# Kernel tuning notes

Hardware: AMD Instinct MI355X
Metric: run time of the kernel (lower is better)

## Reference

```python
import jax, jax.numpy as jnp
import numpy as np
import math

B, IN_CH, IMG = 32, 3, 128
D, L, H, MLP, P = 512, 8, 8, 2048, 8
HD = D // H
EPS = 1e-5


def _conv(x, w, b, stride, pad):
    y = jax.lax.conv_general_dilated(x, w, (stride, stride), pad,
                                     dimension_numbers=("NCHW", "OIHW", "NCHW"))
    return y + b[None, :, None, None]


def _gn(x, g, b, groups):
    Bn, C, Hh, W = x.shape
    xr = x.reshape(Bn, groups, C // groups, Hh, W)
    m = jnp.mean(xr, axis=(2, 3, 4), keepdims=True)
    v = jnp.var(xr, axis=(2, 3, 4), keepdims=True)
    xr = (xr - m) / jnp.sqrt(v + EPS)
    return xr.reshape(Bn, C, Hh, W) * g[None, :, None, None] + b[None, :, None, None]


def _ln(x, g, b):
    m = jnp.mean(x, axis=-1, keepdims=True)
    v = jnp.var(x, axis=-1, keepdims=True)
    return (x - m) / jnp.sqrt(v + EPS) * g + b


def _rot_half(x):
    # interleaved pairs: (x0,x1) -> (-x1,x0)
    x1, x2 = x[..., 0::2], x[..., 1::2]
    return jnp.stack((-x2, x1), axis=-1).reshape(x.shape)


def _xpos_tables(n_pos, hd):
    # faithful to rotary_embedding_torch with use_xpos=True, scale_base=512
    inv = 1.0 / (10000.0 ** (jnp.arange(0, hd, 2, dtype=jnp.float32) / hd))
    seq = jnp.arange(n_pos, dtype=jnp.float32)
    freqs = jnp.repeat(seq[:, None] * inv[None, :], 2, axis=-1)  # (n_pos, hd) interleaved
    sv = (jnp.arange(0, hd, 2, dtype=jnp.float32) + 0.4 * hd) / (1.4 * hd)
    power = (seq - n_pos // 2) / 512.0
    scale = sv[None, :] ** power[:, None]                        # (n_pos, hd//2)
    scale = jnp.concatenate([scale, scale], axis=-1)             # library uses cat, not interleave
    return jnp.cos(freqs), jnp.sin(freqs), scale


def _pos2d(N, Dd):
    g = int(math.isqrt(N))
    y = jnp.tile(jnp.arange(g), g).astype(jnp.float32)
    x = jnp.repeat(jnp.arange(g), g).astype(jnp.float32)
    dq = Dd // 4
    omega = jnp.exp(jnp.arange(dq, dtype=jnp.float32) * -(math.log(10000.0) / dq))
    px, py = x[:, None] * omega, y[:, None] * omega
    return jnp.concatenate([jnp.sin(px), jnp.cos(px), jnp.sin(py), jnp.cos(py)], axis=-1)[None]


def setup_inputs() -> dict:
    key = jax.random.key(0)
    ks = iter(jax.random.split(key, 40))
    def rn(shape, s=0.02):
        return jax.random.normal(next(ks), shape, jnp.float32) * s
    return dict(
        x=jax.random.normal(next(ks), (B, IN_CH, IMG, IMG), jnp.float32),
        conv1_w=rn((32, 3, 3, 3)), conv1_b=jnp.zeros((32,), jnp.float32),
        gn1_g=jnp.ones((32,), jnp.float32), gn1_b=jnp.zeros((32,), jnp.float32),
        conv2_w=rn((64, 32, 3, 3)), conv2_b=jnp.zeros((64,), jnp.float32),
        gn2_g=jnp.ones((64,), jnp.float32), gn2_b=jnp.zeros((64,), jnp.float32),
        patch_w=rn((D, 64, P, P)), patch_b=jnp.zeros((D,), jnp.float32),
        cls_token=rn((1, 1, D), 1.0),
        ln1_g=jnp.ones((L, D), jnp.float32), ln1_b=jnp.zeros((L, D), jnp.float32),
        qkv_w=rn((L, D, 3 * D)), qkv_b=jnp.zeros((L, 3 * D), jnp.float32),
        out_w=rn((L, D, D)), out_b=jnp.zeros((L, D), jnp.float32),
        ln2_g=jnp.ones((L, D), jnp.float32), ln2_b=jnp.zeros((L, D), jnp.float32),
        w1_w=rn((L, D, MLP)), w1_b=jnp.zeros((L, MLP), jnp.float32),
        w2_w=rn((L, D, MLP)), w2_b=jnp.zeros((L, MLP), jnp.float32),
        w3_w=rn((L, MLP, D)), w3_b=jnp.zeros((L, D), jnp.float32),
        fn_g=jnp.ones((D,), jnp.float32), fn_b=jnp.zeros((D,), jnp.float32),
    )


def _forward(x, conv1_w, conv1_b, gn1_g, gn1_b, conv2_w, conv2_b, gn2_g, gn2_b,
             patch_w, patch_b, cls_token, ln1_g, ln1_b, qkv_w, qkv_b, out_w, out_b,
             ln2_g, ln2_b, w1_w, w1_b, w2_w, w2_b, w3_w, w3_b, fn_g, fn_b):
    # conv stem (no downsample)
    f = jax.nn.gelu(_gn(_conv(x, conv1_w, conv1_b, 1, [(1, 1), (1, 1)]), gn1_g, gn1_b, 4), approximate=False)
    f = jax.nn.gelu(_gn(_conv(f, conv2_w, conv2_b, 1, [(1, 1), (1, 1)]), gn2_g, gn2_b, 8), approximate=False)
    # patch embed
    p = _conv(f, patch_w, patch_b, P, "VALID")            # (B, D, g, g)
    Bn, Dd, gh, gw = p.shape
    tokens = p.reshape(Bn, Dd, gh * gw).transpose(0, 2, 1)  # (B, N, D)
    tokens = tokens + _pos2d(gh * gw, Dd)
    xa = jnp.concatenate([jnp.broadcast_to(cls_token, (Bn, 1, Dd)), tokens], axis=1)
    # NOTE: original code applies RoPE with seq_dim=-2 on (B,S,H,hd) -> rotation indexed by HEAD axis
    cos, sin, xsc = _xpos_tables(H, HD)
    scale_att = HD ** -0.5
    for i in range(L):
        n = _ln(xa, ln1_g[i], ln1_b[i])
        qkv = (n @ qkv_w[i] + qkv_b[i]).reshape(Bn, -1, 3, H, HD)
        q, k, v = qkv[:, :, 0], qkv[:, :, 1], qkv[:, :, 2]     # (B, S, H, hd)
        q = q * cos * xsc + _rot_half(q) * sin * xsc
        k = k * cos / xsc + _rot_half(k) * sin / xsc
        attn = jax.nn.softmax(jnp.einsum("bihd,bjhd->bhij", q, k) * scale_att, axis=-1)
        y = jnp.einsum("bhij,bjhd->bihd", attn, v).reshape(Bn, -1, Dd)
        xa = xa + y @ out_w[i] + out_b[i]
        n2 = _ln(xa, ln2_g[i], ln2_b[i])
        xa = xa + (jax.nn.silu(n2 @ w1_w[i] + w1_b[i]) * (n2 @ w2_w[i] + w2_b[i])) @ w3_w[i] + w3_b[i]
    return _ln(xa, fn_g, fn_b)


def reference(x, conv1_w, conv1_b, gn1_g, gn1_b, conv2_w, conv2_b, gn2_g, gn2_b,
              patch_w, patch_b, cls_token, ln1_g, ln1_b, qkv_w, qkv_b, out_w, out_b,
              ln2_g, ln2_b, w1_w, w1_b, w2_w, w2_b, w3_w, w3_b, fn_g, fn_b):
    xa = _forward(x, conv1_w, conv1_b, gn1_g, gn1_b, conv2_w, conv2_b, gn2_g, gn2_b,
                  patch_w, patch_b, cls_token, ln1_g, ln1_b, qkv_w, qkv_b, out_w, out_b,
                  ln2_g, ln2_b, w1_w, w1_b, w2_w, w2_b, w3_w, w3_b, fn_g, fn_b)
    return (xa[:, 0], xa[:, 1:])  # (cls, patches); grid_hw is static (16,16)
```

## Files before the change

### kernel.cpp

```cpp
#include <hip/hip_runtime.h>

#define EPSV 1e-5f
typedef unsigned short u16;
typedef short bf16x8 __attribute__((ext_vector_type(8)));
typedef float f32x4 __attribute__((ext_vector_type(4)));

__device__ __forceinline__ float gelu_exact(float x) {
    return 0.5f * x * (1.0f + erff(x * 0.7071067811865475f));
}
__device__ __forceinline__ u16 to_bf(float x) {
    union { float f; unsigned u; } c; c.f = x;
    unsigned r = c.u + 0x7fffu + ((c.u >> 16) & 1u);
    return (u16)(r >> 16);
}
__device__ __forceinline__ float to_f(u16 h) {
    union { unsigned u; float f; } c; c.u = ((unsigned)h) << 16;
    return c.f;
}
__device__ __forceinline__ void gload_lds16(const void* g, void* l) {
    __builtin_amdgcn_global_load_lds((const __attribute__((address_space(1))) unsigned int*)g,
                                     (__attribute__((address_space(3))) unsigned int*)l, 16, 0, 0);
}

__global__ void k_wsfail(float* out) { out[0] = 1.0e9f; }

__global__ void k_zero(float* p, int n) {
    int i = blockIdx.x * 256 + threadIdx.x;
    if (i < n) p[i] = 0.0f;
}

__global__ void k_wt(const float* __restrict__ w, float* __restrict__ wt, int cout, int cin9) {
    int idx = blockIdx.x * 256 + threadIdx.x;
    if (idx < cout * cin9) {
        int co = idx / cin9, k = idx % cin9;
        wt[k * cout + co] = w[idx];
    }
}

__global__ void k_wpack(const float* __restrict__ w, u16* __restrict__ wp) {
    int idx = blockIdx.x * 256 + threadIdx.x;
    if (idx < 18432) {
        int ci = idx & 31, tc = idx >> 5;
        int tap = tc >> 6, co = tc & 63;
        wp[idx] = to_bf(w[co * 288 + ci * 9 + tap]);
    }
}

__global__ void k_pperm(const float* __restrict__ w, u16* __restrict__ wp) {
    int idx = blockIdx.x * 256 + threadIdx.x;
    int cout = idx >> 12, rem = idx & 4095;
    int tap = rem >> 6, ci = rem & 63;
    wp[idx] = to_bf(w[cout * 4096 + ci * 64 + tap]);
}

__global__ void k_biascat(const float* __restrict__ b1, const float* __restrict__ b2,
                          float* __restrict__ o) {
    int idx = blockIdx.x * 256 + threadIdx.x;
    if (idx < 32768) {
        int l = idx >> 12, pc = idx & 4095;
        int chunk = pc >> 4, within = pc & 15;
        int srccol = (chunk >> 1) * 16 + within;
        o[idx] = (chunk & 1) ? b2[l * 2048 + srccol] : b1[l * 2048 + srccol];
    }
}

__global__ void k_tables(float* __restrict__ postab, float* __restrict__ ropetab) {
    int idx = blockIdx.x * 256 + threadIdx.x;
    if (idx < 256 * 512) {
        int p = idx >> 9, j = idx & 511;
        float coord = (j < 256) ? (float)(p >> 4) : (float)(p & 15);
        int jm = j & 127;
        float om = powf(10000.0f, -(float)jm / 128.0f);
        float arg = coord * om;
        postab[idx] = ((j >> 7) & 1) ? cosf(arg) : sinf(arg);
    }
    if (idx < 512) {
        int h = idx >> 6, d = idx & 63;
        float freq = (float)h * powf(10000.0f, -(float)(d >> 1) / 32.0f);
        float sv = (2.0f * (float)(d & 31) + 25.6f) / 89.6f;
        float pw = ((float)h - 4.0f) / 512.0f;
        float sc = powf(sv, pw);
        ropetab[idx * 4 + 0] = cosf(freq);
        ropetab[idx * 4 + 1] = sinf(freq);
        ropetab[idx * 4 + 2] = sc * 0.125f;
        ropetab[idx * 4 + 3] = 1.0f / sc;
    }
}

__global__ void k_cls(const float* __restrict__ cls, float* __restrict__ xa) {
    int idx = blockIdx.x * 256 + threadIdx.x;
    int b = idx >> 9, d = idx & 511;
    xa[(size_t)(b * 257) * 512 + d] = cls[d];
}

__global__ __launch_bounds__(256) void k_wcvtT(const float* __restrict__ src,
                                               u16* __restrict__ dst, int K, int N) {
    __shared__ float s[32][33];
    int z = blockIdx.z;
    src += (size_t)z * K * N;
    dst += (size_t)z * K * N;
    int k0 = blockIdx.y * 32, n0 = blockIdx.x * 32;
    int t = threadIdx.x, r = t >> 3, c4 = (t & 7) * 4;
    float4 v = *(const float4*)&src[(size_t)(k0 + r) * N + n0 + c4];
    s[r][c4 + 0] = v.x; s[r][c4 + 1] = v.y; s[r][c4 + 2] = v.z; s[r][c4 + 3] = v.w;
    __syncthreads();
    ushort4 o;
    o.x = to_bf(s[c4 + 0][r]); o.y = to_bf(s[c4 + 1][r]);
    o.z = to_bf(s[c4 + 2][r]); o.w = to_bf(s[c4 + 3][r]);
    *(ushort4*)&dst[(size_t)(n0 + r) * K + k0 + c4] = o;
}

__global__ __launch_bounds__(256) void k_wcvtT12(const float* __restrict__ s1,
                                                 const float* __restrict__ s2,
                                                 u16* __restrict__ dst, int K, int N) {
    __shared__ float s[32][33];
    int z = blockIdx.z;
    const float* src = z ? s2 : s1;
    int k0 = blockIdx.y * 32, n0 = blockIdx.x * 32;
    int t = threadIdx.x, r = t >> 3, c4 = (t & 7) * 4;
    float4 v = *(const float4*)&src[(size_t)(k0 + r) * N + n0 + c4];
    s[r][c4 + 0] = v.x; s[r][c4 + 1] = v.y; s[r][c4 + 2] = v.z; s[r][c4 + 3] = v.w;
    __syncthreads();
    ushort4 o;
    o.x = to_bf(s[c4 + 0][r]); o.y = to_bf(s[c4 + 1][r]);
    o.z = to_bf(s[c4 + 2][r]); o.w = to_bf(s[c4 + 3][r]);
    int nsrc = n0 + r;
    int p = ((nsrc >> 4) << 5) + (z << 4) + (nsrc & 15);
    *(ushort4*)&dst[(size_t)p * K + k0 + c4] = o;
}

__global__ __launch_bounds__(256) void k_conv1(const float* __restrict__ in,
                                               const float* __restrict__ wt,
                                               const float* __restrict__ bias,
                                               u16* __restrict__ f1n,
                                               float* __restrict__ sacc) {
    __shared__ float s_in[3][18][18];
    __shared__ float rs[4][4], rq[4][4];
    int b = blockIdx.y;
    int tile = blockIdx.x;
    int y0 = (tile >> 3) << 4;
    int x0 = (tile & 7) << 4;
    int tid = threadIdx.x;
    for (int idx = tid; idx < 972; idx += 256) {
        int ci = idx / 324, r = idx % 324;
        int ly = r / 18, lx = r % 18;
        int gy = y0 + ly - 1, gx = x0 + lx - 1;
        float v = 0.0f;
        if (gy >= 0 && gy < 128 && gx >= 0 && gx < 128)
            v = in[((size_t)(b * 3 + ci) * 128 + gy) * 128 + gx];
        s_in[ci][ly][lx] = v;
    }
    __syncthreads();
    int py = tid >> 4, px = tid & 15;
    float acc[32];
#pragma unroll
    for (int co = 0; co < 32; co++) acc[co] = bias[co];
#pragma unroll
    for (int ci = 0; ci < 3; ci++)
#pragma unroll
        for (int dy = 0; dy < 3; dy++)
#pragma unroll
            for (int dx = 0; dx < 3; dx++) {
                float v = s_in[ci][py + dy][px + dx];
                const float* wr = &wt[(ci * 9 + dy * 3 + dx) * 32];
#pragma unroll
                for (int co = 0; co < 32; co++)
                    acc[co] = fmaf(wr[co], v, acc[co]);
            }
    float s[4] = {0.f, 0.f, 0.f, 0.f}, q[4] = {0.f, 0.f, 0.f, 0.f};
    u16 ob[32];
#pragma unroll
    for (int co = 0; co < 32; co++) {
        u16 hv = to_bf(acc[co]);
        ob[co] = hv;
        float v = to_f(hv);
        s[co >> 3] += v;
        q[co >> 3] += v * v;
    }
    int oy = y0 + py, ox = x0 + px;
    u16* dst = f1n + ((size_t)(b * 16384 + oy * 128 + ox) << 5);
#pragma unroll
    for (int i = 0; i < 8; i++)
        *(ushort4*)(dst + i * 4) = make_ushort4(ob[i * 4], ob[i * 4 + 1], ob[i * 4 + 2], ob[i * 4 + 3]);
#pragma unroll
    for (int g = 0; g < 4; g++) {
#pragma unroll
        for (int off = 1; off < 64; off <<= 1) {
            s[g] += __shfl_xor(s[g], off);
            q[g] += __shfl_xor(q[g], off);
        }
    }
    int w = tid >> 6, lane = tid & 63;
    if (lane == 0)
#pragma unroll
        for (int g = 0; g < 4; g++) { rs[g][w] = s[g]; rq[g][w] = q[g]; }
    __syncthreads();
    if (tid < 4) {
        int g = tid;
        float S = rs[g][0] + rs[g][1] + rs[g][2] + rs[g][3];
        float Q = rq[g][0] + rq[g][1] + rq[g][2] + rq[g][3];
        atomicAdd(&sacc[(b * 4 + g) * 2], S);
        atomicAdd(&sacc[(b * 4 + g) * 2 + 1], Q);
    }
}

__global__ void k_gnfin(const float* __restrict__ sacc, float* __restrict__ st, int entries) {
    int i = blockIdx.x * 256 + threadIdx.x;
    if (i < entries) {
        float m = sacc[2 * i] * (1.0f / 131072.0f);
        float var = sacc[2 * i + 1] * (1.0f / 131072.0f) - m * m;
        st[2 * i] = m;
        st[2 * i + 1] = rsqrtf(var + 1e-5f);
    }
}

__global__ void k_gnap(u16* __restrict__ xio, const float* __restrict__ st,
                       const float* __restrict__ gg, const float* __restrict__ bb,
                       int cm, int sh, int gmul) {
    int idx = blockIdx.x * 256 + threadIdx.x;
    long e = (long)idx * 4;
    int c0 = (int)(e & cm);
    int b = (int)(e >> sh);
    int sid = b * gmul + (c0 >> 3);
    float m = st[2 * sid], r = st[2 * sid + 1];
    ushort4 a = *(ushort4*)&xio[e];
    ushort4 o;
    o.x = to_bf(gelu_exact((to_f(a.x) - m) * r * gg[c0 + 0] + bb[c0 + 0]));
    o.y = to_bf(gelu_exact((to_f(a.y) - m) * r * gg[c0 + 1] + bb[c0 + 1]));
    o.z = to_bf(gelu_exact((to_f(a.z) - m) * r * gg[c0 + 2] + bb[c0 + 2]));
    o.w = to_bf(gelu_exact((to_f(a.w) - m) * r * gg[c0 + 3] + bb[c0 + 3]));
    *(ushort4*)&xio[e] = o;
}

__global__ __launch_bounds__(256) void k_conv2m(const u16* __restrict__ f1b,
                                                const u16* __restrict__ wp,
                                                const float* __restrict__ bias,
                                                u16* __restrict__ f2n,
                                                float* __restrict__ sacc) {
    int b = blockIdx.y;
    int tile = blockIdx.x;
    int y0 = (tile >> 3) << 4;
    int x0 = (tile & 7) << 4;
    int tid = threadIdx.x;
    int w = tid >> 6, lane = tid & 63;
    int l15 = lane & 15, l16 = lane >> 4;

    const u16* base = f1b + ((size_t)b << 19);

    f32x4 acc[4][4];
    f32x4 zf = {0.f, 0.f, 0.f, 0.f};
#pragma unroll
    for (int m = 0; m < 4; m++)
#pragma unroll
        for (int n = 0; n < 4; n++) acc[m][n] = zf;
    bf16x8 zb = {0, 0, 0, 0, 0, 0, 0, 0};

#pragma unroll
    for (int tap = 0; tap < 9; tap++) {
        int dy = tap / 3, dx = tap % 3;
        int gx = x0 + l15 + dx - 1;
        bf16x8 af[4], bk[4];
#pragma unroll
        for (int m = 0; m < 4; m++) {
            int gy = y0 + w * 4 + m + dy - 1;
            bool ok = (gy >= 0) && (gy < 128) && (gx >= 0) && (gx < 128);
            int pix = ok ? (gy * 128 + gx) : 0;
            bf16x8 v = *(const bf16x8*)(base + ((size_t)pix << 5) + l16 * 8);
            af[m] = ok ? v : zb;
        }
#pragma unroll
        for (int n = 0; n < 4; n++)
            bk[n] = *(const bf16x8*)&wp[(tap * 64 + n * 16 + l15) * 32 + l16 * 8];
#pragma unroll
        for (int m = 0; m < 4; m++)
#pragma unroll
            for (int n = 0; n < 4; n++)
                acc[m][n] = __builtin_amdgcn_mfma_f32_16x16x32_bf16(af[m], bk[n], acc[m][n], 0, 0, 0);
    }

#pragma unroll
    for (int n = 0; n < 4; n++) {
        int gco = n * 16 + l15;
        float bv = bias[gco];
        float sn = 0.0f, qn = 0.0f;
#pragma unroll
        for (int m = 0; m < 4; m++) {
            int py = w * 4 + m;
#pragma unroll
            for (int r = 0; r < 4; r++) {
                int px = l16 * 4 + r;
                float v = acc[m][n][r] + bv;
                u16 hv = to_bf(v);
                f2n[((size_t)(b * 16384 + (y0 + py) * 128 + x0 + px) << 6) + gco] = hv;
                float vf = to_f(hv);
                sn += vf;
                qn += vf * vf;
            }
        }
#pragma unroll
        for (int off = 1; off <= 4; off <<= 1) { sn += __shfl_xor(sn, off); qn += __shfl_xor(qn, off); }
        sn += __shfl_xor(sn, 16); qn += __shfl_xor(qn, 16);
        sn += __shfl_xor(sn, 32); qn += __shfl_xor(qn, 32);
        if (lane == 0 || lane == 8) {
            int g = n * 2 + (lane >> 3);
            atomicAdd(&sacc[(b * 8 + g) * 2], sn);
            atomicAdd(&sacc[(b * 8 + g) * 2 + 1], qn);
        }
    }
}

template <int MODE, int EPI>
__global__ __launch_bounds__(256) void k_bgemm(const u16* __restrict__ A,
                                               const u16* __restrict__ Bt,
                                               const float* __restrict__ bias,
                                               void* __restrict__ Cp,
                                               const float* __restrict__ aux,
                                               int M, int N, int K) {
    __shared__ u16 ldsA[8192];
    __shared__ u16 ldsB[8192];
    int tid = threadIdx.x;
    int w = tid >> 6, lane = tid & 63;
    int bm = blockIdx.y * 128, bn = blockIdx.x * 128;
    int wr = w >> 1, wc = w & 1;
    int l15 = lane & 15, l16 = lane >> 4;

    f32x4 acc[4][4];
    f32x4 zf = {0.f, 0.f, 0.f, 0.f};
#pragma unroll
    for (int m = 0; m < 4; m++)
#pragma unroll
        for (int n = 0; n < 4; n++) acc[m][n] = zf;

    for (int k0 = 0; k0 < K; k0 += 64) {
#pragma unroll
        for (int i = 0; i < 4; i++) {
            int chunk = (w * 4 + i) * 64 + lane;
            int kg = chunk >> 7, row = chunk & 127;
            const u16* src;
            if (MODE == 0) {
                int grow = bm + row;
                if (grow > M - 1) grow = M - 1;
                src = A + (size_t)grow * K + k0 + kg * 8;
            } else {
                int grow = bm + row;
                int bimg = grow >> 8, p = grow & 255;
                int kga = (k0 >> 3) + kg;
                int tap = kga >> 3, cq = kga & 7;
                int ky = tap >> 3, kx = tap & 7;
                int gy = ((p >> 4) << 3) + ky, gx = ((p & 15) << 3) + kx;
                src = A + (((size_t)(bimg * 16384 + gy * 128 + gx)) << 6) + cq * 8;
            }
            gload_lds16(src, &ldsA[(w * 4 + i) * 512]);
        }
#pragma unroll
        for (int i = 0; i < 4; i++) {
            int chunk = (w * 4 + i) * 64 + lane;
            int col = chunk >> 3, kgs = chunk & 7;
            int kg_src = kgs ^ (col & 7);
            const u16* src = Bt + (size_t)(bn + col) * K + k0 + kg_src * 8;
            gload_lds16(src, &ldsB[(w * 4 + i) * 512]);
        }
        __syncthreads();

        bf16x8 af[4][2], bfr[4][2];
#pragma unroll
        for (int kk = 0; kk < 2; kk++) {
            int kga = kk * 4 + l16;
#pragma unroll
            for (int m = 0; m < 4; m++) {
                int row_l = wr * 64 + m * 16 + l15;
                af[m][kk] = *(const bf16x8*)&ldsA[(kga * 128 + row_l) * 8];
            }
#pragma unroll
            for (int n = 0; n < 4; n++) {
                int col_l = wc * 64 + n * 16 + l15;
                bfr[n][kk] = *(const bf16x8*)&ldsB[(col_l * 8 + (kga ^ (col_l & 7))) * 8];
            }
        }
#pragma unroll
        for (int m = 0; m < 4; m++)
#pragma unroll
            for (int n = 0; n < 4; n++) {
                acc[m][n] = __builtin_amdgcn_mfma_f32_16x16x32_bf16(af[m][0], bfr[n][0], acc[m][n], 0, 0, 0);
                acc[m][n] = __builtin_amdgcn_mfma_f32_16x16x32_bf16(af[m][1], bfr[n][1], acc[m][n], 0, 0, 0);
            }
        __syncthreads();
    }

    if (EPI == 6) {
#pragma unroll
        for (int np = 0; np < 2; np++) {
            int n_a = np * 2, n_b = np * 2 + 1;
            float bva = bias[bn + wc * 64 + n_a * 16 + l15];
            float bvb = bias[bn + wc * 64 + n_b * 16 + l15];
            int ocol = (bn >> 1) + wc * 32 + np * 16 + l15;
#pragma unroll
            for (int m = 0; m < 4; m++) {
#pragma unroll
                for (int r = 0; r < 4; r++) {
                    int grow = bm + wr * 64 + m * 16 + l16 * 4 + r;
                    if (grow < M) {
                        float h1v = to_f(to_bf(acc[m][n_a][r] + bva));
                        float h2v = to_f(to_bf(acc[m][n_b][r] + bvb));
                        float sl = h1v / (1.0f + __expf(-h1v));
                        ((u16*)Cp)[(size_t)grow * (N >> 1) + ocol] = to_bf(sl * h2v);
                    }
                }
            }
        }
    } else {
#pragma unroll
        for (int n = 0; n < 4; n++) {
            int gcol = bn + wc * 64 + n * 16 + l15;
            float bv = bias[gcol];
            float rc = 0.f, rsn = 0.f, rsc = 1.f;
            bool isqk = false, odd = false;
            if (EPI == 7) {
                isqk = gcol < 1024;
                odd = (l15 & 1) != 0;
                const float* rb = &aux[(gcol & 511) * 4];
                if (isqk) {
                    rc = rb[0]; rsn = rb[1];
                    rsc = (gcol < 512) ? rb[2] : rb[3];
                }
            }
#pragma unroll
            for (int m = 0; m < 4; m++) {
#pragma unroll
                for (int r = 0; r < 4; r++) {
                    int grow = bm + wr * 64 + m * 16 + l16 * 4 + r;
                    float v = acc[m][n][r] + bv;
                    if (EPI == 7) {
                        float p = __shfl_xor(v, 1);
                        float vr = isqk ? ((odd ? (v * rc + p * rsn) : (v * rc - p * rsn)) * rsc) : v;
                        if (grow < M) ((u16*)Cp)[(size_t)grow * N + gcol] = to_bf(vr);
                    } else if (EPI == 1) {
                        if (grow < M) ((float*)Cp)[(size_t)grow * N + gcol] = v;
                    } else if (EPI == 2) {
                        if (grow < M) ((float*)Cp)[(size_t)grow * N + gcol] += v;
                    } else {
                        int bimg = grow >> 8, p2 = grow & 255;
                        v += aux[p2 * 512 + gcol];
                        ((float*)Cp)[((size_t)(bimg * 257) + 1 + p2) * 512 + gcol] = v;
                    }
                }
            }
        }
    }
}

__global__ __launch_bounds__(256) void k_lnb(const float* __restrict__ x,
                                             const float* __restrict__ g,
                                             const float* __restrict__ bta,
                                             u16* __restrict__ o) {
    int row = blockIdx.x * 4 + (threadIdx.x >> 6);
    int lane = threadIdx.x & 63;
    const float4* xr = (const float4*)(x + (size_t)row * 512);
    float4 a = xr[lane * 2], b = xr[lane * 2 + 1];
    float s = a.x + a.y + a.z + a.w + b.x + b.y + b.z + b.w;
#pragma unroll
    for (int off = 1; off < 64; off <<= 1) s += __shfl_xor(s, off);
    float mean = s * (1.0f / 512.0f);
    float d[8] = {a.x - mean, a.y - mean, a.z - mean, a.w - mean,
                  b.x - mean, b.y - mean, b.z - mean, b.w - mean};
    float q = 0.0f;
#pragma unroll
    for (int i = 0; i < 8; i++) q += d[i] * d[i];
#pragma unroll
    for (int off = 1; off < 64; off <<= 1) q += __shfl_xor(q, off);
    float rstd = rsqrtf(q * (1.0f / 512.0f) + EPSV);
    int c0 = lane * 8;
    float4 g0 = *(const float4*)&g[c0], g1 = *(const float4*)&g[c0 + 4];
    float4 b0 = *(const float4*)&bta[c0], b1 = *(const float4*)&bta[c0 + 4];
    u16* orow = o + (size_t)row * 512 + c0;
    *(ushort4*)orow = make_ushort4(to_bf(d[0] * rstd * g0.x + b0.x), to_bf(d[1] * rstd * g0.y + b0.y),
                                   to_bf(d[2] * rstd * g0.z + b0.z), to_bf(d[3] * rstd * g0.w + b0.w));
    *(ushort4*)(orow + 4) = make_ushort4(to_bf(d[4] * rstd * g1.x + b1.x), to_bf(d[5] * rstd * g1.y + b1.y),
                                         to_bf(d[6] * rstd * g1.z + b1.z), to_bf(d[7] * rstd * g1.w + b1.w));
}

__global__ __launch_bounds__(256) void k_ln_out(const float* __restrict__ x,
                                                const float* __restrict__ g,
                                                const float* __restrict__ bta,
                                                float* __restrict__ out) {
    int row = blockIdx.x * 4 + (threadIdx.x >> 6);
    int lane = threadIdx.x & 63;
    const float4* xr = (const float4*)(x + (size_t)row * 512);
    float4 a = xr[lane * 2], b = xr[lane * 2 + 1];
    float s = a.x + a.y + a.z + a.w + b.x + b.y + b.z + b.w;
#pragma unroll
    for (int off = 1; off < 64; off <<= 1) s += __shfl_xor(s, off);
    float mean = s * (1.0f / 512.0f);
    float d[8] = {a.x - mean, a.y - mean, a.z - mean, a.w - mean,
                  b.x - mean, b.y - mean, b.z - mean, b.w - mean};
    float q = 0.0f;
#pragma unroll
    for (int i = 0; i < 8; i++) q += d[i] * d[i];
#pragma unroll
    for (int off = 1; off < 64; off <<= 1) q += __shfl_xor(q, off);
    float rstd = rsqrtf(q * (1.0f / 512.0f) + EPSV);
    int bb = row / 257, t = row % 257;
    float* dst = (t == 0) ? out + (size_t)bb * 512
                          : out + 16384 + (size_t)(bb * 256 + (t - 1)) * 512;
    int c0 = lane * 8;
    float4 g0 = *(const float4*)&g[c0], g1 = *(const float4*)&g[c0 + 4];
    float4 b0 = *(const float4*)&bta[c0], b1 = *(const float4*)&bta[c0 + 4];
    *(float4*)(dst + c0) = make_float4(d[0] * rstd * g0.x + b0.x, d[1] * rstd * g0.y + b0.y,
                                       d[2] * rstd * g0.z + b0.z, d[3] * rstd * g0.w + b0.w);
    *(float4*)(dst + c0 + 4) = make_float4(d[4] * rstd * g1.x + b1.x, d[5] * rstd * g1.y + b1.y,
                                           d[6] * rstd * g1.z + b1.z, d[7] * rstd * g1.w + b1.w);
}

__global__ __launch_bounds__(256) void k_attn_mfma(const u16* __restrict__ qkv,
                                                   u16* __restrict__ y) {
    __shared__ u16 KV[64][72];
    __shared__ float sc[32][260];
    __shared__ u16 Pb[32][328];
    __shared__ float red1[32][8];
    __shared__ float red2[32][8];
    __shared__ float invr[32];

    int bid = blockIdx.x;
    int qt = bid % 9, bh = bid / 9;
    int h = bh & 7, b = bh >> 3;
    int q0 = qt * 32;
    int tid = threadIdx.x;
    int w = tid >> 6, lane = tid & 63;
    int l15 = lane & 15, l16 = lane >> 4;

    bf16x8 aq[2][2];
#pragma unroll
    for (int m = 0; m < 2; m++) {
        int grow = q0 + m * 16 + l15; if (grow > 256) grow = 256;
        const u16* qp = qkv + (size_t)(b * 257 + grow) * 1536 + h * 64 + l16 * 8;
        aq[m][0] = *(const bf16x8*)qp;
        aq[m][1] = *(const bf16x8*)(qp + 32);
    }

    for (int t = 0; t < 5; t++) {
        int j0 = t * 64;
        int gk = j0 + w * 16 + l15; if (gk > 256) gk = 256;
        const u16* kp = qkv + (size_t)(b * 257 + gk) * 1536 + 512 + h * 64 + l16 * 8;
        bf16x8 bk0 = *(const bf16x8*)kp;
        bf16x8 bk1 = *(const bf16x8*)(kp + 32);
        f32x4 a2[2];
        f32x4 zf = {0.f, 0.f, 0.f, 0.f};
#pragma unroll
        for (int m = 0; m < 2; m++) {
            a2[m] = zf;
            a2[m] = __builtin_amdgcn_mfma_f32_16x16x32_bf16(aq[m][0], bk0, a2[m], 0, 0, 0);
            a2[m] = __builtin_amdgcn_mfma_f32_16x16x32_bf16(aq[m][1], bk1, a2[m], 0, 0, 0);
        }
        int col = j0 + w * 16 + l15;
        if (col < 257) {
#pragma unroll
            for (int m = 0; m < 2; m++)
#pragma unroll
                for (int r = 0; r < 4; r++)
                    sc[m * 16 + l16 * 4 + r][col] = a2[m][r];
        }
    }
    __syncthreads();

    {
        int r = tid >> 3, sub = tid & 7;
        float mx = -1e30f;
        for (int j = sub; j < 257; j += 8) mx = fmaxf(mx, sc[r][j]);
        red1[r][sub] = mx;
        __syncthreads();
        mx = red1[r][0];
#pragma unroll
        for (int i = 1; i < 8; i++) mx = fmaxf(mx, red1[r][i]);
        float sm = 0.0f;
        for (int j = sub; j < 257; j += 8) {
            float e = __expf(sc[r][j] - mx);
            Pb[r][j] = to_bf(e);
            sm += e;
        }
        for (int j = 257 + sub; j < 320; j += 8) Pb[r][j] = 0;
        red2[r][sub] = sm;
        __syncthreads();
        if (sub == 0) {
            float t = red2[r][0];
#pragma unroll
            for (int i = 1; i < 8; i++) t += red2[r][i];
            invr[r] = 1.0f / t;
        }
        __syncthreads();
    }

    f32x4 oacc[2];
    {
        f32x4 zf = {0.f, 0.f, 0.f, 0.f};
        oacc[0] = zf; oacc[1] = zf;
    }
    for (int t = 0; t < 5; t++) {
        int j0 = t * 64;
        {
            int vk = tid & 63, vd0 = (tid >> 6) * 16;
            int gk = j0 + vk;
            u16 o[16];
            if (gk <= 256) {
                const u16* vp = qkv + (size_t)(b * 257 + gk) * 1536 + 1024 + h * 64 + vd0;
                ushort4 a0 = *(const ushort4*)vp, a1 = *(const ushort4*)(vp + 4);
                ushort4 a2v = *(const ushort4*)(vp + 8), a3 = *(const ushort4*)(vp + 12);
                o[0] = a0.x; o[1] = a0.y; o[2] = a0.z; o[3] = a0.w;
                o[4] = a1.x; o[5] = a1.y; o[6] = a1.z; o[7] = a1.w;
                o[8] = a2v.x; o[9] = a2v.y; o[10] = a2v.z; o[11] = a2v.w;
                o[12] = a3.x; o[13] = a3.y; o[14] = a3.z; o[15] = a3.w;
            } else {
#pragma unroll
                for (int i = 0; i < 16; i++) o[i] = 0;
            }
#pragma unroll
            for (int i = 0; i < 16; i++) KV[vd0 + i][vk] = o[i];
        }
        __syncthreads();

        bf16x8 ap[2][2], bv[2];
#pragma unroll
        for (int m = 0; m < 2; m++)
#pragma unroll
            for (int kk = 0; kk < 2; kk++)
                ap[m][kk] = *(const bf16x8*)&Pb[m * 16 + l15][j0 + kk * 32 + l16 * 8];
#pragma unroll
        for (int kk = 0; kk < 2; kk++)
            bv[kk] = *(const bf16x8*)&KV[w * 16 + l15][kk * 32 + l16 * 8];
#pragma unroll
        for (int m = 0; m < 2; m++) {
            oacc[m] = __builtin_amdgcn_mfma_f32_16x16x32_bf16(ap[m][0], bv[0], oacc[m], 0, 0, 0);
            oacc[m] = __builtin_amdgcn_mfma_f32_16x16x32_bf16(ap[m][1], bv[1], oacc[m], 0, 0, 0);
        }
        __syncthreads();
    }

#pragma unroll
    for (int m = 0; m < 2; m++)
#pragma unroll
        for (int r = 0; r < 4; r++) {
            int lr = m * 16 + l16 * 4 + r;
            int grow = q0 + lr;
            if (grow < 257)
                y[(size_t)(b * 257 + grow) * 512 + h * 64 + w * 16 + l15] =
                    to_bf(oacc[m][r] * invr[lr]);
        }
}

extern "C" void kernel_launch(void* const* d_in, const int* in_sizes, int n_in,
                              void* d_out, int out_size, void* d_ws, size_t ws_size,
                              hipStream_t stream) {
    const float* x       = (const float*)d_in[0];
    const float* conv1_w = (const float*)d_in[1];
    const float* conv1_b = (const float*)d_in[2];
    const float* gn1_g   = (const float*)d_in[3];
    const float* gn1_b   = (const float*)d_in[4];
    const float* conv2_w = (const float*)d_in[5];
    const float* conv2_b = (const float*)d_in[6];
    const float* gn2_g   = (const float*)d_in[7];
    const float* gn2_b   = (const float*)d_in[8];
    const float* patch_w = (const float*)d_in[9];
    const float* patch_b = (const float*)d_in[10];
    const float* cls_tok = (const float*)d_in[11];
    const float* ln1_g   = (const float*)d_in[12];
    const float* ln1_b   = (const float*)d_in[13];
    const float* qkv_w   = (const float*)d_in[14];
    const float* qkv_b   = (const float*)d_in[15];
    const float* out_w   = (const float*)d_in[16];
    const float* out_b   = (const float*)d_in[17];
    const float* ln2_g   = (const float*)d_in[18];
    const float* ln2_b   = (const float*)d_in[19];
    const float* w1_w    = (const float*)d_in[20];
    const float* w1_b    = (const float*)d_in[21];
    const float* w2_w    = (const float*)d_in[22];
    const float* w2_b    = (const float*)d_in[23];
    const float* w3_w    = (const float*)d_in[24];
    const float* w3_b    = (const float*)d_in[25];
    const float* fn_g    = (const float*)d_in[26];
    const float* fn_b    = (const float*)d_in[27];
    float* out = (float*)d_out;
    char* wsb  = (char*)d_ws;

    const size_t O_R1    = 0;
    const size_t O_HB    = O_R1 + 67371008;
    const size_t O_NB    = O_R1 + 101056512;
    const size_t O_Y     = O_R1 + 109477888;
    const size_t O_R2    = 134217728;
    const size_t O_XA    = 201326592;
    const size_t O_PWT   = 218169344;
    const size_t O_QKVT  = 222363648;
    const size_t O_OUTT  = 234946560;
    const size_t O_WL    = 239140864;
    const size_t O_PT    = 245432320;
    const size_t O_RT    = 245956608;
    const size_t O_CW1   = 245964800;
    const size_t O_CW2   = 245968896;
    const size_t O_ST    = 246042624;
    const size_t O_SA    = 246046720;
    const size_t O_B12   = 246050816;
    const size_t NEED    = 246181888;
    if (ws_size < NEED) {
        k_wsfail<<<1, 1, 0, stream>>>(out);
        return;
    }
    u16*   f2n    = (u16*)(wsb + O_R1);
    u16*   hb     = (u16*)(wsb + O_HB);
    u16*   nb     = (u16*)(wsb + O_NB);
    u16*   yb     = (u16*)(wsb + O_Y);
    u16*   f1n    = (u16*)(wsb + O_R2);
    u16*   qkvb   = (u16*)(wsb + O_R2);
    float* xa     = (float*)(wsb + O_XA);
    u16*   patchT = (u16*)(wsb + O_PWT);
    u16*   qkvT   = (u16*)(wsb + O_QKVT);
    u16*   outT   = (u16*)(wsb + O_OUTT);
    u16*   w12Tl  = (u16*)(wsb + O_WL);
    u16*   w3Tl   = (u16*)(wsb + O_WL + 4194304);
    float* postab = (float*)(wsb + O_PT);
    float* ropet  = (float*)(wsb + O_RT);
    float* w1t    = (float*)(wsb + O_CW1);
    u16*   wpack  = (u16*)(wsb + O_CW2);
    float* stat   = (float*)(wsb + O_ST);
    float* sacc   = (float*)(wsb + O_SA);
    float* bias12 = (float*)(wsb + O_B12);

    k_zero<<<3, 256, 0, stream>>>(sacc, 768);
    k_wt<<<4, 256, 0, stream>>>(conv1_w, w1t, 32, 27);
    k_wpack<<<72, 256, 0, stream>>>(conv2_w, wpack);
    k_tables<<<512, 256, 0, stream>>>(postab, ropet);
    k_pperm<<<8192, 256, 0, stream>>>(patch_w, patchT);
    k_biascat<<<128, 256, 0, stream>>>(w1_b, w2_b, bias12);
    k_wcvtT<<<dim3(48, 16, 8), 256, 0, stream>>>(qkv_w, qkvT, 512, 1536);
    k_wcvtT<<<dim3(16, 16, 8), 256, 0, stream>>>(out_w, outT, 512, 512);

    k_conv1<<<dim3(64, 32), 256, 0, stream>>>(x, w1t, conv1_b, f1n, sacc);
    k_gnfin<<<1, 256, 0, stream>>>(sacc, stat, 128);
    k_gnap<<<16384, 256, 0, stream>>>(f1n, stat, gn1_g, gn1_b, 31, 19, 4);
    k_conv2m<<<dim3(64, 32), 256, 0, stream>>>(f1n, wpack, conv2_b, f2n, sacc + 256);
    k_gnfin<<<1, 256, 0, stream>>>(sacc + 256, stat + 256, 256);
    k_gnap<<<32768, 256, 0, stream>>>(f2n, stat + 256, gn2_g, gn2_b, 63, 20, 8);

    k_bgemm<1, 3><<<dim3(4, 64), 256, 0, stream>>>(f2n, patchT, patch_b, xa, postab, 8192, 512, 4096);
    k_cls<<<64, 256, 0, stream>>>(cls_tok, xa);

    for (int l = 0; l < 8; l++) {
        k_wcvtT12<<<dim3(64, 16, 2), 256, 0, stream>>>(w1_w + (size_t)l * 1048576,
                                                       w2_w + (size_t)l * 1048576, w12Tl, 512, 2048);
        k_wcvtT<<<dim3(16, 64, 1), 256, 0, stream>>>(w3_w + (size_t)l * 1048576, w3Tl, 2048, 512);

        k_lnb<<<2056, 256, 0, stream>>>(xa, ln1_g + l * 512, ln1_b + l * 512, nb);
        k_bgemm<0, 7><<<dim3(12, 65), 256, 0, stream>>>(nb, qkvT + (size_t)l * 786432,
                                                        qkv_b + l * 1536, qkvb, ropet, 8224, 1536, 512);
        k_attn_mfma<<<2304, 256, 0, stream>>>(qkvb, yb);
        k_bgemm<0, 2><<<dim3(4, 65), 256, 0, stream>>>(yb, outT + (size_t)l * 262144,
                                                       out_b + l * 512, xa, nullptr, 8224, 512, 512);
        k_lnb<<<2056, 256, 0, stream>>>(xa, ln2_g + l * 512, ln2_b + l * 512, nb);
        k_bgemm<0, 6><<<dim3(32, 65), 256, 0, stream>>>(nb, w12Tl,
                                                        bias12 + l * 4096, hb, nullptr, 8224, 4096, 512);
        k_bgemm<0, 2><<<dim3(4, 65), 256, 0, stream>>>(hb, w3Tl,
                                                       w3_b + l * 512, xa, nullptr, 8224, 512, 2048);
    }
    k_ln_out<<<2056, 256, 0, stream>>>(xa, fn_g, fn_b, out);
}
```

Measured before the change: 2.596 ms.

## Merge setup kernels, batch MLP weight conversion, double-buffer attention V tile

```diff
diff --git a/kernel.cpp b/kernel.cpp
--- a/kernel.cpp
+++ b/kernel.cpp
@@ -24,49 +24,15 @@
 
 __global__ void k_wsfail(float* out) { out[0] = 1.0e9f; }
 
-__global__ void k_zero(float* p, int n) {
-    int i = blockIdx.x * 256 + threadIdx.x;
-    if (i < n) p[i] = 0.0f;
-}
-
-__global__ void k_wt(const float* __restrict__ w, float* __restrict__ wt, int cout, int cin9) {
+__global__ void k_setup(float* __restrict__ sacc,
+                        const float* __restrict__ conv1_w, float* __restrict__ w1t,
+                        const float* __restrict__ conv2_w, u16* __restrict__ wpack,
+                        const float* __restrict__ b1, const float* __restrict__ b2,
+                        float* __restrict__ bias12,
+                        float* __restrict__ postab, float* __restrict__ ropetab,
+                        const float* __restrict__ cls, float* __restrict__ xa) {
     int idx = blockIdx.x * 256 + threadIdx.x;
-    if (idx < cout * cin9) {
-        int co = idx / cin9, k = idx % cin9;
-        wt[k * cout + co] = w[idx];
-    }
-}
-
-__global__ void k_wpack(const float* __restrict__ w, u16* __restrict__ wp) {
-    int idx = blockIdx.x * 256 + threadIdx.x;
-    if (idx < 18432) {
-        int ci = idx & 31, tc = idx >> 5;
-        int tap = tc >> 6, co = tc & 63;
-        wp[idx] = to_bf(w[co * 288 + ci * 9 + tap]);
-    }
-}
-
-__global__ void k_pperm(const float* __restrict__ w, u16* __restrict__ wp) {
-    int idx = blockIdx.x * 256 + threadIdx.x;
-    int cout = idx >> 12, rem = idx & 4095;
-    int tap = rem >> 6, ci = rem & 63;
-    wp[idx] = to_bf(w[cout * 4096 + ci * 64 + tap]);
-}
-
-__global__ void k_biascat(const float* __restrict__ b1, const float* __restrict__ b2,
-                          float* __restrict__ o) {
-    int idx = blockIdx.x * 256 + threadIdx.x;
-    if (idx < 32768) {
-        int l = idx >> 12, pc = idx & 4095;
-        int chunk = pc >> 4, within = pc & 15;
-        int srccol = (chunk >> 1) * 16 + within;
-        o[idx] = (chunk & 1) ? b2[l * 2048 + srccol] : b1[l * 2048 + srccol];
-    }
-}
-
-__global__ void k_tables(float* __restrict__ postab, float* __restrict__ ropetab) {
-    int idx = blockIdx.x * 256 + threadIdx.x;
-    if (idx < 256 * 512) {
+    if (idx < 131072) {
         int p = idx >> 9, j = idx & 511;
         float coord = (j < 256) ? (float)(p >> 4) : (float)(p & 15);
         int jm = j & 127;
@@ -85,12 +51,33 @@
         ropetab[idx * 4 + 2] = sc * 0.125f;
         ropetab[idx * 4 + 3] = 1.0f / sc;
     }
-}
-
-__global__ void k_cls(const float* __restrict__ cls, float* __restrict__ xa) {
+    if (idx < 768) sacc[idx] = 0.0f;
+    if (idx < 864) {
+        int co = idx / 27, k = idx % 27;
+        w1t[k * 32 + co] = conv1_w[idx];
+    }
+    if (idx < 18432) {
+        int ci = idx & 31, tc = idx >> 5;
+        int tap = tc >> 6, co = tc & 63;
+        wpack[idx] = to_bf(conv2_w[co * 288 + ci * 9 + tap]);
+    }
+    if (idx < 32768) {
+        int l = idx >> 12, pc = idx & 4095;
+        int chunk = pc >> 4, within = pc & 15;
+        int srccol = (chunk >> 1) * 16 + within;
+        bias12[idx] = (chunk & 1) ? b2[l * 2048 + srccol] : b1[l * 2048 + srccol];
+    }
+    if (idx < 16384) {
+        int b = idx >> 9, d = idx & 511;
+        xa[(size_t)(b * 257) * 512 + d] = cls[d];
+    }
+}
+
+__global__ void k_pperm(const float* __restrict__ w, u16* __restrict__ wp) {
     int idx = blockIdx.x * 256 + threadIdx.x;
-    int b = idx >> 9, d = idx & 511;
-    xa[(size_t)(b * 257) * 512 + d] = cls[d];
+    int cout = idx >> 12, rem = idx & 4095;
+    int tap = rem >> 6, ci = rem & 63;
+    wp[idx] = to_bf(w[cout * 4096 + ci * 64 + tap]);
 }
 
 __global__ __launch_bounds__(256) void k_wcvtT(const float* __restrict__ src,
@@ -110,23 +97,25 @@
     *(ushort4*)&dst[(size_t)(n0 + r) * K + k0 + c4] = o;
 }
 
-__global__ __launch_bounds__(256) void k_wcvtT12(const float* __restrict__ s1,
-                                                 const float* __restrict__ s2,
-                                                 u16* __restrict__ dst, int K, int N) {
+__global__ __launch_bounds__(256) void k_wcvtT12L(const float* __restrict__ w1,
+                                                  const float* __restrict__ w2,
+                                                  u16* __restrict__ w12All) {
     __shared__ float s[32][33];
     int z = blockIdx.z;
-    const float* src = z ? s2 : s1;
+    int layer = z >> 1, sel = z & 1;
+    const float* src = (sel ? w2 : w1) + (size_t)layer * 1048576;
+    u16* dst = w12All + (size_t)layer * 2097152;
     int k0 = blockIdx.y * 32, n0 = blockIdx.x * 32;
     int t = threadIdx.x, r = t >> 3, c4 = (t & 7) * 4;
-    float4 v = *(const float4*)&src[(size_t)(k0 + r) * N + n0 + c4];
+    float4 v = *(const float4*)&src[(size_t)(k0 + r) * 2048 + n0 + c4];
     s[r][c4 + 0] = v.x; s[r][c4 + 1] = v.y; s[r][c4 + 2] = v.z; s[r][c4 + 3] = v.w;
     __syncthreads();
     ushort4 o;
     o.x = to_bf(s[c4 + 0][r]); o.y = to_bf(s[c4 + 1][r]);
     o.z = to_bf(s[c4 + 2][r]); o.w = to_bf(s[c4 + 3][r]);
     int nsrc = n0 + r;
-    int p = ((nsrc >> 4) << 5) + (z << 4) + (nsrc & 15);
-    *(ushort4*)&dst[(size_t)p * K + k0 + c4] = o;
+    int p = ((nsrc >> 4) << 5) + (sel << 4) + (nsrc & 15);
+    *(ushort4*)&dst[(size_t)p * 512 + k0 + c4] = o;
 }
 
 __global__ __launch_bounds__(256) void k_conv1(const float* __restrict__ in,
@@ -204,17 +193,7 @@
     }
 }
 
-__global__ void k_gnfin(const float* __restrict__ sacc, float* __restrict__ st, int entries) {
-    int i = blockIdx.x * 256 + threadIdx.x;
-    if (i < entries) {
-        float m = sacc[2 * i] * (1.0f / 131072.0f);
-        float var = sacc[2 * i + 1] * (1.0f / 131072.0f) - m * m;
-        st[2 * i] = m;
-        st[2 * i + 1] = rsqrtf(var + 1e-5f);
-    }
-}
-
-__global__ void k_gnap(u16* __restrict__ xio, const float* __restrict__ st,
+__global__ void k_gnap(u16* __restrict__ xio, const float* __restrict__ sacc,
                        const float* __restrict__ gg, const float* __restrict__ bb,
                        int cm, int sh, int gmul) {
     int idx = blockIdx.x * 256 + threadIdx.x;
@@ -222,7 +201,9 @@
     int c0 = (int)(e & cm);
     int b = (int)(e >> sh);
     int sid = b * gmul + (c0 >> 3);
-    float m = st[2 * sid], r = st[2 * sid + 1];
+    float m = sacc[2 * sid] * (1.0f / 131072.0f);
+    float var = sacc[2 * sid + 1] * (1.0f / 131072.0f) - m * m;
+    float r = rsqrtf(var + 1e-5f);
     ushort4 a = *(ushort4*)&xio[e];
     ushort4 o;
     o.x = to_bf(gelu_exact((to_f(a.x) - m) * r * gg[c0 + 0] + bb[c0 + 0]));
@@ -513,7 +494,7 @@
 
 __global__ __launch_bounds__(256) void k_attn_mfma(const u16* __restrict__ qkv,
                                                    u16* __restrict__ y) {
-    __shared__ u16 KV[64][72];
+    __shared__ u16 KV[2][64][72];
     __shared__ float sc[32][260];
     __shared__ u16 Pb[32][328];
     __shared__ float red1[32][8];
@@ -596,6 +577,7 @@
     }
     for (int t = 0; t < 5; t++) {
         int j0 = t * 64;
+        int buf = t & 1;
         {
             int vk = tid & 63, vd0 = (tid >> 6) * 16;
             int gk = j0 + vk;
@@ -613,7 +595,7 @@
                 for (int i = 0; i < 16; i++) o[i] = 0;
             }
 #pragma unroll
-            for (int i = 0; i < 16; i++) KV[vd0 + i][vk] = o[i];
+            for (int i = 0; i < 16; i++) KV[buf][vd0 + i][vk] = o[i];
         }
         __syncthreads();
 
@@ -625,13 +607,12 @@
                 ap[m][kk] = *(const bf16x8*)&Pb[m * 16 + l15][j0 + kk * 32 + l16 * 8];
 #pragma unroll
         for (int kk = 0; kk < 2; kk++)
-            bv[kk] = *(const bf16x8*)&KV[w * 16 + l15][kk * 32 + l16 * 8];
+            bv[kk] = *(const bf16x8*)&KV[buf][w * 16 + l15][kk * 32 + l16 * 8];
 #pragma unroll
         for (int m = 0; m < 2; m++) {
             oacc[m] = __builtin_amdgcn_mfma_f32_16x16x32_bf16(ap[m][0], bv[0], oacc[m], 0, 0, 0);
             oacc[m] = __builtin_amdgcn_mfma_f32_16x16x32_bf16(ap[m][1], bv[1], oacc[m], 0, 0, 0);
         }
-        __syncthreads();
     }
 
 #pragma unroll
@@ -681,6 +662,8 @@
     char* wsb  = (char*)d_ws;
 
     const size_t O_R1    = 0;
+    const size_t O_W12A  = 0;
+    const size_t O_W3A   = 33554432;
     const size_t O_HB    = O_R1 + 67371008;
     const size_t O_NB    = O_R1 + 101056512;
     const size_t O_Y     = O_R1 + 109477888;
@@ -689,12 +672,10 @@
     const size_t O_PWT   = 218169344;
     const size_t O_QKVT  = 222363648;
     const size_t O_OUTT  = 234946560;
-    const size_t O_WL    = 239140864;
     const size_t O_PT    = 245432320;
     const size_t O_RT    = 245956608;
     const size_t O_CW1   = 245964800;
     const size_t O_CW2   = 245968896;
-    const size_t O_ST    = 246042624;
     const size_t O_SA    = 246046720;
     const size_t O_B12   = 246050816;
     const size_t NEED    = 246181888;
@@ -703,6 +684,8 @@
         return;
     }
     u16*   f2n    = (u16*)(wsb + O_R1);
+    u16*   w12All = (u16*)(wsb + O_W12A);
+    u16*   w3All  = (u16*)(wsb + O_W3A);
     u16*   hb     = (u16*)(wsb + O_HB);
     u16*   nb     = (u16*)(wsb + O_NB);
     u16*   yb     = (u16*)(wsb + O_Y);
@@ -712,40 +695,30 @@
     u16*   patchT = (u16*)(wsb + O_PWT);
     u16*   qkvT   = (u16*)(wsb + O_QKVT);
     u16*   outT   = (u16*)(wsb + O_OUTT);
-    u16*   w12Tl  = (u16*)(wsb + O_WL);
-    u16*   w3Tl   = (u16*)(wsb + O_WL + 4194304);
     float* postab = (float*)(wsb + O_PT);
     float* ropet  = (float*)(wsb + O_RT);
     float* w1t    = (float*)(wsb + O_CW1);
     u16*   wpack  = (u16*)(wsb + O_CW2);
-    float* stat   = (float*)(wsb + O_ST);
     float* sacc   = (float*)(wsb + O_SA);
     float* bias12 = (float*)(wsb + O_B12);
 
-    k_zero<<<3, 256, 0, stream>>>(sacc, 768);
-    k_wt<<<4, 256, 0, stream>>>(conv1_w, w1t, 32, 27);
-    k_wpack<<<72, 256, 0, stream>>>(conv2_w, wpack);
-    k_tables<<<512, 256, 0, stream>>>(postab, ropet);
+    k_setup<<<512, 256, 0, stream>>>(sacc, conv1_w, w1t, conv2_w, wpack,
+                                     w1_b, w2_b, bias12, postab, ropet, cls_tok, xa);
     k_pperm<<<8192, 256, 0, stream>>>(patch_w, patchT);
-    k_biascat<<<128, 256, 0, stream>>>(w1_b, w2_b, bias12);
     k_wcvtT<<<dim3(48, 16, 8), 256, 0, stream>>>(qkv_w, qkvT, 512, 1536);
     k_wcvtT<<<dim3(16, 16, 8), 256, 0, stream>>>(out_w, outT, 512, 512);
 
     k_conv1<<<dim3(64, 32), 256, 0, stream>>>(x, w1t, conv1_b, f1n, sacc);
-    k_gnfin<<<1, 256, 0, stream>>>(sacc, stat, 128);
-    k_gnap<<<16384, 256, 0, stream>>>(f1n, stat, gn1_g, gn1_b, 31, 19, 4);
+    k_gnap<<<16384, 256, 0, stream>>>(f1n, sacc, gn1_g, gn1_b, 31, 19, 4);
     k_conv2m<<<dim3(64, 32), 256, 0, stream>>>(f1n, wpack, conv2_b, f2n, sacc + 256);
-    k_gnfin<<<1, 256, 0, stream>>>(sacc + 256, stat + 256, 256);
-    k_gnap<<<32768, 256, 0, stream>>>(f2n, stat + 256, gn2_g, gn2_b, 63, 20, 8);
+    k_gnap<<<32768, 256, 0, stream>>>(f2n, sacc + 256, gn2_g, gn2_b, 63, 20, 8);
 
     k_bgemm<1, 3><<<dim3(4, 64), 256, 0, stream>>>(f2n, patchT, patch_b, xa, postab, 8192, 512, 4096);
-    k_cls<<<64, 256, 0, stream>>>(cls_tok, xa);
+
+    k_wcvtT12L<<<dim3(64, 16, 16), 256, 0, stream>>>(w1_w, w2_w, w12All);
+    k_wcvtT<<<dim3(16, 64, 8), 256, 0, stream>>>(w3_w, w3All, 2048, 512);
 
     for (int l = 0; l < 8; l++) {
-        k_wcvtT12<<<dim3(64, 16, 2), 256, 0, stream>>>(w1_w + (size_t)l * 1048576,
-                                                       w2_w + (size_t)l * 1048576, w12Tl, 512, 2048);
-        k_wcvtT<<<dim3(16, 64, 1), 256, 0, stream>>>(w3_w + (size_t)l * 1048576, w3Tl, 2048, 512);
-
         k_lnb<<<2056, 256, 0, stream>>>(xa, ln1_g + l * 512, ln1_b + l * 512, nb);
         k_bgemm<0, 7><<<dim3(12, 65), 256, 0, stream>>>(nb, qkvT + (size_t)l * 786432,
                                                         qkv_b + l * 1536, qkvb, ropet, 8224, 1536, 512);
@@ -753,9 +726,9 @@
         k_bgemm<0, 2><<<dim3(4, 65), 256, 0, stream>>>(yb, outT + (size_t)l * 262144,
                                                        out_b + l * 512, xa, nullptr, 8224, 512, 512);
         k_lnb<<<2056, 256, 0, stream>>>(xa, ln2_g + l * 512, ln2_b + l * 512, nb);
-        k_bgemm<0, 6><<<dim3(32, 65), 256, 0, stream>>>(nb, w12Tl,
+        k_bgemm<0, 6><<<dim3(32, 65), 256, 0, stream>>>(nb, w12All + (size_t)l * 2097152,
                                                         bias12 + l * 4096, hb, nullptr, 8224, 4096, 512);
-        k_bgemm<0, 2><<<dim3(4, 65), 256, 0, stream>>>(hb, w3Tl,
+        k_bgemm<0, 2><<<dim3(4, 65), 256, 0, stream>>>(hb, w3All + (size_t)l * 1048576,
                                                        w3_b + l * 512, xa, nullptr, 8224, 512, 2048);
     }
     k_ln_out<<<2056, 256, 0, stream>>>(xa, fn_g, fn_b, out);
```

Result: no change. 2.556 ms (-1.5%).
